# Optimization experiments

Hardware: AMD Instinct MI355X
Metric: run time of the kernel (lower is better)

## Reference

```python
import jax, jax.numpy as jnp
import numpy as np

B, C, H, W = 4, 256, 64, 64
DQK = C // 4


def setup_inputs() -> dict:
    key = jax.random.key(0)
    ks = jax.random.split(key, 5)
    s = 0.05
    x = jax.random.normal(ks[0], (B, C, H, W), dtype=jnp.float32)
    Wq = jax.random.normal(ks[1], (DQK, C), dtype=jnp.float32) * s
    Wk = jax.random.normal(ks[2], (DQK, C), dtype=jnp.float32) * s
    Wv = jax.random.normal(ks[3], (C, C), dtype=jnp.float32) * s
    bq = jnp.zeros((DQK,), jnp.float32)
    bk = jnp.zeros((DQK,), jnp.float32)
    bv = jnp.zeros((C,), jnp.float32)
    gamma = jnp.zeros((1,), jnp.float32)
    return {"x": x, "Wq": Wq, "bq": bq, "Wk": Wk, "bk": bk,
            "Wv": Wv, "bv": bv, "gamma": gamma}


def reference(x, Wq, bq, Wk, bk, Wv, bv, gamma):
    b, c, h, w = x.shape
    n = h * w
    xf = x.reshape(b, c, n)                      # [B, C, N]
    # 1x1 convs == per-pixel linear projections
    q = jnp.einsum('dc,bcn->bnd', Wq, xf) + bq   # [B, N, Dqk]
    k = jnp.einsum('dc,bcn->bdn', Wk, xf) + bk[None, :, None]  # [B, Dqk, N]
    v = jnp.einsum('ec,bcn->ben', Wv, xf) + bv[None, :, None]  # [B, C, N]
    energy = jnp.einsum('bnd,bdm->bnm', q, k)    # [B, N, N]
    attn = jax.nn.softmax(energy, axis=-1)       # softmax over keys
    # out[b,c,i] = sum_j v[b,c,j] * attn[b,i,j]
    out = jnp.einsum('bcj,bij->bci', v, attn)    # [B, C, N]
    out = out.reshape(b, c, h, w)
    return gamma * out + x
```

## Files before the change

kernel.cpp:

```cpp
#include <hip/hip_runtime.h>

#define B_ 4
#define C_ 256
#define N_ 4096
#define D_ 64

typedef __bf16 bf16x8 __attribute__((ext_vector_type(8)));
typedef float floatx4 __attribute__((ext_vector_type(4)));
typedef unsigned short ushort8v __attribute__((ext_vector_type(8)));
typedef unsigned short ushort4v __attribute__((ext_vector_type(4)));
typedef unsigned short ushort2v __attribute__((ext_vector_type(2)));

static __device__ __forceinline__ unsigned short f2bf(float f) {
    unsigned int u = __builtin_bit_cast(unsigned int, f);
    u += 0x7fffu + ((u >> 16) & 1u);
    return (unsigned short)(u >> 16);
}
static __device__ __forceinline__ float bf2f(unsigned short h) {
    unsigned int u = ((unsigned int)h) << 16;
    return __builtin_bit_cast(float, u);
}
static __device__ __forceinline__ unsigned int cvt_pk_bf16(float lo, float hi) {
    unsigned int d;
    asm("v_cvt_pk_bf16_f32 %0, %1, %2" : "=v"(d) : "v"(lo), "v"(hi));
    return d;
}

#define GLOAD16(gp, lp)                                                      \
    __builtin_amdgcn_global_load_lds(                                        \
        (const __attribute__((address_space(1))) void*)(gp),                 \
        (__attribute__((address_space(3))) void*)(lp), 16, 0, 0)

__global__ __launch_bounds__(256, 2) void proj_kernel(
    const float* __restrict__ x,
    const float* __restrict__ Wq, const float* __restrict__ Wk,
    const float* __restrict__ Wv,
    const float* __restrict__ bq, const float* __restrict__ bk,
    const float* __restrict__ bv,
    unsigned short* __restrict__ Qg, unsigned short* __restrict__ Kg,
    unsigned short* __restrict__ Vg)
{
    __shared__ __align__(16) unsigned short xs[64 * 264];
    __shared__ __align__(16) unsigned short Lt[128 * 72];

    const int n0 = blockIdx.x * 64;
    const int b  = blockIdx.y;
    const int t  = threadIdx.x;
    const int w  = t >> 6;
    const int lane = t & 63;
    const int g  = lane >> 4;
    const int m  = lane & 15;

#pragma unroll
    for (int k = 0; k < 8; ++k) {
        int e  = t + 256 * k;
        int cp = e >> 4;
        int c  = 2 * cp;
        int n4 = (e & 15) * 4;
        float4 v0 = *(const float4*)(x + ((size_t)b*C_ + c    )*N_ + n0 + n4);
        float4 v1 = *(const float4*)(x + ((size_t)b*C_ + c + 1)*N_ + n0 + n4);
        float a0[4] = {v0.x, v0.y, v0.z, v0.w};
        float a1[4] = {v1.x, v1.y, v1.z, v1.w};
#pragma unroll
        for (int j = 0; j < 4; ++j) {
            int n = n4 + j;
            unsigned int u = cvt_pk_bf16(a0[j], a1[j]);
            *(unsigned int*)&xs[n*264 + (((c >> 3) ^ (n & 7)) << 3) + (c & 7)] = u;
        }
    }
    __syncthreads();

#pragma unroll
    for (int s = 0; s < 3; ++s) {
        const int f0 = 128 * s;

        float bias_[2][4];
#pragma unroll
        for (int mt = 0; mt < 2; ++mt)
#pragma unroll
            for (int r = 0; r < 4; ++r) {
                int fg = f0 + 32*w + 16*mt + 4*g + r;
                bias_[mt][r] = (fg < 64) ? bq[fg]
                             : (fg < 128) ? bk[fg - 64] : bv[fg - 128];
            }

        const int fr0 = f0 + 32*w + m;
        const int fr1 = fr0 + 16;
        const float* wr0 = (fr0 < 64) ? Wq + (size_t)fr0*C_
                         : (fr0 < 128)? Wk + (size_t)(fr0 - 64)*C_
                                      : Wv + (size_t)(fr0 - 128)*C_;
        const float* wr1 = (fr1 < 64) ? Wq + (size_t)fr1*C_
                         : (fr1 < 128)? Wk + (size_t)(fr1 - 64)*C_
                                      : Wv + (size_t)(fr1 - 128)*C_;
        bf16x8 afr[2][8];
#pragma unroll
        for (int ks = 0; ks < 8; ++ks) {
            float4 l0 = *(const float4*)(wr0 + 32*ks + 8*g);
            float4 h0 = *(const float4*)(wr0 + 32*ks + 8*g + 4);
            float4 l1 = *(const float4*)(wr1 + 32*ks + 8*g);
            float4 h1 = *(const float4*)(wr1 + 32*ks + 8*g + 4);
            uint4 u0, u1;
            u0.x = cvt_pk_bf16(l0.x, l0.y); u0.y = cvt_pk_bf16(l0.z, l0.w);
            u0.z = cvt_pk_bf16(h0.x, h0.y); u0.w = cvt_pk_bf16(h0.z, h0.w);
            u1.x = cvt_pk_bf16(l1.x, l1.y); u1.y = cvt_pk_bf16(l1.z, l1.w);
            u1.z = cvt_pk_bf16(h1.x, h1.y); u1.w = cvt_pk_bf16(h1.z, h1.w);
            afr[0][ks] = __builtin_bit_cast(bf16x8, u0);
            afr[1][ks] = __builtin_bit_cast(bf16x8, u1);
        }

        floatx4 acc[2][4];
#pragma unroll
        for (int mt = 0; mt < 2; ++mt)
#pragma unroll
            for (int nt = 0; nt < 4; ++nt)
                acc[mt][nt] = (floatx4){0.f,0.f,0.f,0.f};

#pragma unroll
        for (int ks = 0; ks < 8; ++ks) {
#pragma unroll
            for (int nt = 0; nt < 4; ++nt) {
                int n = 16*nt + m;
                bf16x8 bfr = *(const bf16x8*)
                    &xs[n*264 + (((4*ks + g) ^ (n & 7)) << 3)];
#pragma unroll
                for (int mt = 0; mt < 2; ++mt)
                    acc[mt][nt] = __builtin_amdgcn_mfma_f32_16x16x32_bf16(
                                      afr[mt][ks], bfr, acc[mt][nt], 0, 0, 0);
            }
        }

#pragma unroll
        for (int mt = 0; mt < 2; ++mt)
#pragma unroll
            for (int nt = 0; nt < 4; ++nt)
#pragma unroll
                for (int r = 0; r < 4; ++r)
                    Lt[(32*w + 16*mt + 4*g + r)*72 + 16*nt + m] =
                        f2bf(acc[mt][nt][r] + bias_[mt][r]);
        __syncthreads();

        if (s == 0) {
#pragma unroll
            for (int k = 0; k < 4; ++k) {
                int e   = t + 256 * k;
                int fq0 = (e >> 6) * 8;
                int nl  = e & 63;
                ushort8v u;
#pragma unroll
                for (int j = 0; j < 8; ++j) u[j] = Lt[(fq0 + j)*72 + nl];
                unsigned short* dst = (fq0 < 64)
                    ? (Qg + ((size_t)b*N_ + n0 + nl)*D_ + fq0)
                    : (Kg + ((size_t)b*N_ + n0 + nl)*D_ + (fq0 - 64));
                *(ushort8v*)dst = u;
            }
        } else {
            const int cb = (s - 1) * 128;
#pragma unroll
            for (int k = 0; k < 4; ++k) {
                int e  = t + 256 * k;
                int fr = e >> 3;
                int n8 = (e & 7) * 8;
                ushort8v u = *(const ushort8v*)&Lt[fr*72 + n8];
                *(ushort8v*)(Vg + ((size_t)b*C_ + cb + fr)*N_ + n0 + n8) = u;
            }
        }
        __syncthreads();
    }
}

__global__ __launch_bounds__(512, 2) void flash_kernel(
    const unsigned short* __restrict__ Qg, const unsigned short* __restrict__ Kg,
    const unsigned short* __restrict__ Vg,
    unsigned short* __restrict__ Opart, float* __restrict__ ML)
{
    __shared__ __align__(16) unsigned short Vlds[32 * 512];
    __shared__ __align__(16) unsigned short Klds[2][8 * 512];
    __shared__ __align__(16) unsigned short PA[16 * 64 * 8];
    __shared__ float AL[128];

    const int g8   = blockIdx.x;
    const int tile = blockIdx.y;
    const int half = g8 & 1;
    const int b    = g8 >> 1;
    const int n0   = tile * 128;
    const int t    = threadIdx.x;
    const int w    = t >> 6;
    const int lane = t & 63;
    const int g    = lane >> 4;
    const int m    = lane & 15;
    const int wq   = w >> 2;
    const int cq   = w & 3;

    const unsigned short* Qb = Qg + ((size_t)b*N_ + n0)*D_;
    const unsigned short* Kb = Kg + (size_t)b*N_*D_;
    const unsigned short* Vb = Vg + (size_t)b*C_*N_;

    const int cstart = half * 32;
    const int cend   = cstart + 32;

    bf16x8 qf[2];
#pragma unroll
    for (int ks = 0; ks < 2; ++ks)
        qf[ks] = *(const bf16x8*)(Qb + (size_t)(16*w + m)*D_ + 32*ks + 8*g);

    floatx4 accO[4][4];
#pragma unroll
    for (int rt = 0; rt < 4; ++rt)
#pragma unroll
        for (int ct = 0; ct < 4; ++ct)
            accO[rt][ct] = (floatx4){0.f, 0.f, 0.f, 0.f};

    float mrow = -1e30f, lrow = 0.f;

    {
        const unsigned short* gp =
            Kb + (size_t)(cstart*64 + 16*(w >> 1) + m)*D_ + 32*(w & 1) + 8*g;
        GLOAD16(gp, &Klds[0][w * 512]);
    }
    __syncthreads();

    for (int t64 = cstart; t64 < cend; ++t64) {
        const int j0 = t64 * 64;
        const int kb = (t64 - cstart) & 1;

#pragma unroll
        for (int u = 0; u < 4; ++u) {
            int sidx = 4*w + u;
            int ks   = sidx >> 4;
            int cb   = sidx & 15;
            const unsigned short* gp =
                Vb + (size_t)(16*cb + m)*N_ + j0 + 32*ks + 8*g;
            GLOAD16(gp, &Vlds[sidx * 512]);
        }
        if (t64 + 1 < cend) {
            const unsigned short* gp =
                Kb + (size_t)((t64+1)*64 + 16*(w >> 1) + m)*D_
                   + 32*(w & 1) + 8*g;
            GLOAD16(gp, &Klds[kb ^ 1][w * 512]);
        }

        floatx4 accST[4];
#pragma unroll
        for (int jt = 0; jt < 4; ++jt) accST[jt] = (floatx4){0.f,0.f,0.f,0.f};
#pragma unroll
        for (int ks = 0; ks < 2; ++ks)
#pragma unroll
            for (int jt = 0; jt < 4; ++jt) {
                bf16x8 kfr = *(const bf16x8*)
                    &Klds[kb][(jt*2 + ks)*512 + lane*8];
                accST[jt] = __builtin_amdgcn_mfma_f32_16x16x32_bf16(
                                kfr, qf[ks], accST[jt], 0, 0, 0);
            }

        float mx = -1e30f;
#pragma unroll
        for (int jt = 0; jt < 4; ++jt)
#pragma unroll
            for (int r = 0; r < 4; ++r) mx = fmaxf(mx, accST[jt][r]);
        mx = fmaxf(mx, __shfl_xor(mx, 16));
        mx = fmaxf(mx, __shfl_xor(mx, 32));
        float mnew  = fmaxf(mrow, mx);
        float alpha = __expf(mrow - mnew);
        mrow = mnew;
        float p[4][4];
        float rs = 0.f;
#pragma unroll
        for (int jt = 0; jt < 4; ++jt)
#pragma unroll
            for (int r = 0; r < 4; ++r) {
                float e = __expf(accST[jt][r] - mnew);
                p[jt][r] = e;
                rs += e;
            }
        rs += __shfl_xor(rs, 16);
        rs += __shfl_xor(rs, 32);
        lrow = lrow * alpha + rs;

        if (g == 0) AL[16*w + m] = alpha;

#pragma unroll
        for (int jt = 0; jt < 4; ++jt) {
            uint2 pu;
            pu.x = cvt_pk_bf16(p[jt][0], p[jt][1]);
            pu.y = cvt_pk_bf16(p[jt][2], p[jt][3]);
            int frag = (w*2 + (jt >> 1))*64 + 16*(2*(jt & 1) + (g >> 1)) + m;
            *(uint2*)&PA[frag*8 + 4*(g & 1)] = pu;
        }

        __syncthreads();

#pragma unroll
        for (int rt = 0; rt < 4; ++rt) {
            floatx4 a4 = *(const floatx4*)&AL[64*wq + 16*rt + 4*g];
#pragma unroll
            for (int ct = 0; ct < 4; ++ct)
                accO[rt][ct] *= a4;
        }
#pragma unroll
        for (int ks = 0; ks < 2; ++ks) {
            bf16x8 pf[4];
#pragma unroll
            for (int rt = 0; rt < 4; ++rt)
                pf[rt] = *(const bf16x8*)
                    &PA[((8*wq + rt*2 + ks)*64 + lane)*8];
#pragma unroll
            for (int ct = 0; ct < 4; ++ct) {
                int sidx = ks*16 + 4*cq + ct;
                bf16x8 vfrag = *(const bf16x8*)&Vlds[sidx*512 + lane*8];
#pragma unroll
                for (int rt = 0; rt < 4; ++rt)
                    accO[rt][ct] = __builtin_amdgcn_mfma_f32_16x16x32_bf16(
                                       pf[rt], vfrag, accO[rt][ct], 0, 0, 0);
            }
        }

        __syncthreads();
    }

    const size_t tbase = ((size_t)(half*B_ + b)*32 + tile);
    unsigned short* Ob = Opart + tbase * (C_ * 128);
    float* ml = ML + tbase * 256;

    if (g == 0) {
        ml[16*w + m]       = mrow;
        ml[128 + 16*w + m] = lrow;
    }

#pragma unroll
    for (int rt = 0; rt < 4; ++rt)
#pragma unroll
        for (int ct = 0; ct < 4; ++ct) {
            int c  = 64*cq + 16*ct + m;
            int q0 = 64*wq + 16*rt + 4*g;
            uint2 pu;
            pu.x = cvt_pk_bf16(accO[rt][ct][0], accO[rt][ct][1]);
            pu.y = cvt_pk_bf16(accO[rt][ct][2], accO[rt][ct][3]);
            *(uint2*)(Ob + (size_t)c*128 + q0) = pu;
        }
}

__global__ __launch_bounds__(256) void combine_kernel(
    const unsigned short* __restrict__ Opart, const float* __restrict__ ML,
    const float* __restrict__ x, const float* __restrict__ gamma,
    float* __restrict__ out)
{
    __shared__ float sc0[128], sc1[128];
    const int tile   = blockIdx.x;
    const int cslice = blockIdx.y;
    const int b      = blockIdx.z;
    const int n0     = tile * 128;
    const int t      = threadIdx.x;

    if (t < 128) {
        const float* ml0 = ML + ((size_t)(0*B_ + b)*32 + tile)*256;
        const float* ml1 = ML + ((size_t)(1*B_ + b)*32 + tile)*256;
        float m0 = ml0[t], l0 = ml0[128 + t];
        float m1 = ml1[t], l1 = ml1[128 + t];
        float M  = fmaxf(m0, m1);
        float f0 = __expf(m0 - M), f1 = __expf(m1 - M);
        float L  = f0*l0 + f1*l1;
        float gm = gamma[0];
        sc0[t] = gm * f0 / L;
        sc1[t] = gm * f1 / L;
    }
    __syncthreads();

    const int nq = t & 31;
    const int cl = t >> 5;
    const float* xb = x   + (size_t)b*C_*N_;
    float*       ob = out + (size_t)b*C_*N_;
    const unsigned short* O0 = Opart + ((size_t)(0*B_ + b)*32 + tile)*(C_*128);
    const unsigned short* O1 = Opart + ((size_t)(1*B_ + b)*32 + tile)*(C_*128);

    float s0[4], s1[4];
#pragma unroll
    for (int k = 0; k < 4; ++k) { s0[k] = sc0[4*nq + k]; s1[k] = sc1[4*nq + k]; }

#pragma unroll
    for (int i = 0; i < 4; ++i) {
        int c = 32*cslice + 8*i + cl;
        float4 x4 = *(const float4*)(xb + (size_t)c*N_ + n0 + 4*nq);
        ushort4v a4 = *(const ushort4v*)(O0 + (size_t)c*128 + 4*nq);
        ushort4v b4 = *(const ushort4v*)(O1 + (size_t)c*128 + 4*nq);
        float4 y;
        y.x = s0[0]*bf2f(a4[0]) + s1[0]*bf2f(b4[0]) + x4.x;
        y.y = s0[1]*bf2f(a4[1]) + s1[1]*bf2f(b4[1]) + x4.y;
        y.z = s0[2]*bf2f(a4[2]) + s1[2]*bf2f(b4[2]) + x4.z;
        y.w = s0[3]*bf2f(a4[3]) + s1[3]*bf2f(b4[3]) + x4.w;
        *(float4*)(ob + (size_t)c*N_ + n0 + 4*nq) = y;
    }
}

extern "C" void kernel_launch(void* const* d_in, const int* in_sizes, int n_in,
                              void* d_out, int out_size, void* d_ws, size_t ws_size,
                              hipStream_t stream) {
    const float* x     = (const float*)d_in[0];
    const float* Wq    = (const float*)d_in[1];
    const float* bq    = (const float*)d_in[2];
    const float* Wk    = (const float*)d_in[3];
    const float* bk    = (const float*)d_in[4];
    const float* Wv    = (const float*)d_in[5];
    const float* bv    = (const float*)d_in[6];
    const float* gamma = (const float*)d_in[7];
    float* out = (float*)d_out;

    unsigned short* Qg = (unsigned short*)d_ws;
    unsigned short* Kg = Qg + (size_t)B_*N_*D_;
    unsigned short* Vg = Kg + (size_t)B_*N_*D_;
    unsigned short* Op = Vg + (size_t)B_*C_*N_;
    float* ML = (float*)(Op + (size_t)2*B_*32*C_*128);

    proj_kernel<<<dim3(64, 4), 256, 0, stream>>>(x, Wq, Wk, Wv,
                                                 bq, bk, bv, Qg, Kg, Vg);
    flash_kernel<<<dim3(8, 32), 512, 0, stream>>>(Qg, Kg, Vg, Op, ML);
    combine_kernel<<<dim3(32, 8, 4), 256, 0, stream>>>(Op, ML, x, gamma, out);
}
```

Baseline: 186.9 us.

## Rework flash attention with 32x32 MFMA tiles, 4-way key split, double-buffered V

```diff
diff --git a/kernel.cpp b/kernel.cpp
--- a/kernel.cpp
+++ b/kernel.cpp
@@ -7,6 +7,7 @@
 
 typedef __bf16 bf16x8 __attribute__((ext_vector_type(8)));
 typedef float floatx4 __attribute__((ext_vector_type(4)));
+typedef float floatx16 __attribute__((ext_vector_type(16)));
 typedef unsigned short ushort8v __attribute__((ext_vector_type(8)));
 typedef unsigned short ushort4v __attribute__((ext_vector_type(4)));
 typedef unsigned short ushort2v __attribute__((ext_vector_type(2)));
@@ -31,7 +32,7 @@
         (const __attribute__((address_space(1))) void*)(gp),                 \
         (__attribute__((address_space(3))) void*)(lp), 16, 0, 0)
 
-__global__ __launch_bounds__(256, 2) void proj_kernel(
+__global__ __launch_bounds__(256, 3) void proj_kernel(
     const float* __restrict__ x,
     const float* __restrict__ Wq, const float* __restrict__ Wk,
     const float* __restrict__ Wv,
@@ -40,11 +41,13 @@
     unsigned short* __restrict__ Qg, unsigned short* __restrict__ Kg,
     unsigned short* __restrict__ Vg)
 {
-    __shared__ __align__(16) unsigned short xs[64 * 264];
-    __shared__ __align__(16) unsigned short Lt[128 * 72];
+    __shared__ __align__(16) unsigned short smem[64 * 264];
+    unsigned short* xs = smem;
+    unsigned short* Lt = smem;
 
     const int n0 = blockIdx.x * 64;
-    const int b  = blockIdx.y;
+    const int f0 = blockIdx.y * 128;
+    const int b  = blockIdx.z;
     const int t  = threadIdx.x;
     const int w  = t >> 6;
     const int lane = t & 63;
@@ -68,103 +71,99 @@
             *(unsigned int*)&xs[n*264 + (((c >> 3) ^ (n & 7)) << 3) + (c & 7)] = u;
         }
     }
+
+    float bias_[2][4];
+#pragma unroll
+    for (int mt = 0; mt < 2; ++mt)
+#pragma unroll
+        for (int r = 0; r < 4; ++r) {
+            int fg = f0 + 32*w + 16*mt + 4*g + r;
+            bias_[mt][r] = (fg < 64) ? bq[fg]
+                         : (fg < 128) ? bk[fg - 64] : bv[fg - 128];
+        }
+
+    const int fr0 = f0 + 32*w + m;
+    const int fr1 = fr0 + 16;
+    const float* wr0 = (fr0 < 64) ? Wq + (size_t)fr0*C_
+                     : (fr0 < 128)? Wk + (size_t)(fr0 - 64)*C_
+                                  : Wv + (size_t)(fr0 - 128)*C_;
+    const float* wr1 = (fr1 < 64) ? Wq + (size_t)fr1*C_
+                     : (fr1 < 128)? Wk + (size_t)(fr1 - 64)*C_
+                                  : Wv + (size_t)(fr1 - 128)*C_;
+    bf16x8 afr[2][8];
+#pragma unroll
+    for (int ks = 0; ks < 8; ++ks) {
+        float4 l0 = *(const float4*)(wr0 + 32*ks + 8*g);
+        float4 h0 = *(const float4*)(wr0 + 32*ks + 8*g + 4);
+        float4 l1 = *(const float4*)(wr1 + 32*ks + 8*g);
+        float4 h1 = *(const float4*)(wr1 + 32*ks + 8*g + 4);
+        uint4 u0, u1;
+        u0.x = cvt_pk_bf16(l0.x, l0.y); u0.y = cvt_pk_bf16(l0.z, l0.w);
+        u0.z = cvt_pk_bf16(h0.x, h0.y); u0.w = cvt_pk_bf16(h0.z, h0.w);
+        u1.x = cvt_pk_bf16(l1.x, l1.y); u1.y = cvt_pk_bf16(l1.z, l1.w);
+        u1.z = cvt_pk_bf16(h1.x, h1.y); u1.w = cvt_pk_bf16(h1.z, h1.w);
+        afr[0][ks] = __builtin_bit_cast(bf16x8, u0);
+        afr[1][ks] = __builtin_bit_cast(bf16x8, u1);
+    }
+
+    floatx4 acc[2][4];
+#pragma unroll
+    for (int mt = 0; mt < 2; ++mt)
+#pragma unroll
+        for (int nt = 0; nt < 4; ++nt) acc[mt][nt] = (floatx4){0.f,0.f,0.f,0.f};
+
     __syncthreads();
 
 #pragma unroll
-    for (int s = 0; s < 3; ++s) {
-        const int f0 = 128 * s;
-
-        float bias_[2][4];
-#pragma unroll
-        for (int mt = 0; mt < 2; ++mt)
-#pragma unroll
-            for (int r = 0; r < 4; ++r) {
-                int fg = f0 + 32*w + 16*mt + 4*g + r;
-                bias_[mt][r] = (fg < 64) ? bq[fg]
-                             : (fg < 128) ? bk[fg - 64] : bv[fg - 128];
-            }
-
-        const int fr0 = f0 + 32*w + m;
-        const int fr1 = fr0 + 16;
-        const float* wr0 = (fr0 < 64) ? Wq + (size_t)fr0*C_
-                         : (fr0 < 128)? Wk + (size_t)(fr0 - 64)*C_
-                                      : Wv + (size_t)(fr0 - 128)*C_;
-        const float* wr1 = (fr1 < 64) ? Wq + (size_t)fr1*C_
-                         : (fr1 < 128)? Wk + (size_t)(fr1 - 64)*C_
-                                      : Wv + (size_t)(fr1 - 128)*C_;
-        bf16x8 afr[2][8];
-#pragma unroll
-        for (int ks = 0; ks < 8; ++ks) {
-            float4 l0 = *(const float4*)(wr0 + 32*ks + 8*g);
-            float4 h0 = *(const float4*)(wr0 + 32*ks + 8*g + 4);
-            float4 l1 = *(const float4*)(wr1 + 32*ks + 8*g);
-            float4 h1 = *(const float4*)(wr1 + 32*ks + 8*g + 4);
-            uint4 u0, u1;
-            u0.x = cvt_pk_bf16(l0.x, l0.y); u0.y = cvt_pk_bf16(l0.z, l0.w);
-            u0.z = cvt_pk_bf16(h0.x, h0.y); u0.w = cvt_pk_bf16(h0.z, h0.w);
-            u1.x = cvt_pk_bf16(l1.x, l1.y); u1.y = cvt_pk_bf16(l1.z, l1.w);
-            u1.z = cvt_pk_bf16(h1.x, h1.y); u1.w = cvt_pk_bf16(h1.z, h1.w);
-            afr[0][ks] = __builtin_bit_cast(bf16x8, u0);
-            afr[1][ks] = __builtin_bit_cast(bf16x8, u1);
-        }
-
-        floatx4 acc[2][4];
-#pragma unroll
-        for (int mt = 0; mt < 2; ++mt)
-#pragma unroll
-            for (int nt = 0; nt < 4; ++nt)
-                acc[mt][nt] = (floatx4){0.f,0.f,0.f,0.f};
-
-#pragma unroll
-        for (int ks = 0; ks < 8; ++ks) {
-#pragma unroll
-            for (int nt = 0; nt < 4; ++nt) {
-                int n = 16*nt + m;
-                bf16x8 bfr = *(const bf16x8*)
-                    &xs[n*264 + (((4*ks + g) ^ (n & 7)) << 3)];
-#pragma unroll
-                for (int mt = 0; mt < 2; ++mt)
-                    acc[mt][nt] = __builtin_amdgcn_mfma_f32_16x16x32_bf16(
-                                      afr[mt][ks], bfr, acc[mt][nt], 0, 0, 0);
-            }
-        }
-
-#pragma unroll
-        for (int mt = 0; mt < 2; ++mt)
-#pragma unroll
-            for (int nt = 0; nt < 4; ++nt)
-#pragma unroll
-                for (int r = 0; r < 4; ++r)
-                    Lt[(32*w + 16*mt + 4*g + r)*72 + 16*nt + m] =
-                        f2bf(acc[mt][nt][r] + bias_[mt][r]);
-        __syncthreads();
-
-        if (s == 0) {
-#pragma unroll
-            for (int k = 0; k < 4; ++k) {
-                int e   = t + 256 * k;
-                int fq0 = (e >> 6) * 8;
-                int nl  = e & 63;
-                ushort8v u;
-#pragma unroll
-                for (int j = 0; j < 8; ++j) u[j] = Lt[(fq0 + j)*72 + nl];
-                unsigned short* dst = (fq0 < 64)
-                    ? (Qg + ((size_t)b*N_ + n0 + nl)*D_ + fq0)
-                    : (Kg + ((size_t)b*N_ + n0 + nl)*D_ + (fq0 - 64));
-                *(ushort8v*)dst = u;
-            }
-        } else {
-            const int cb = (s - 1) * 128;
-#pragma unroll
-            for (int k = 0; k < 4; ++k) {
-                int e  = t + 256 * k;
-                int fr = e >> 3;
-                int n8 = (e & 7) * 8;
-                ushort8v u = *(const ushort8v*)&Lt[fr*72 + n8];
-                *(ushort8v*)(Vg + ((size_t)b*C_ + cb + fr)*N_ + n0 + n8) = u;
-            }
-        }
-        __syncthreads();
+    for (int ks = 0; ks < 8; ++ks) {
+#pragma unroll
+        for (int nt = 0; nt < 4; ++nt) {
+            int n = 16*nt + m;
+            bf16x8 bfr = *(const bf16x8*)
+                &xs[n*264 + (((4*ks + g) ^ (n & 7)) << 3)];
+#pragma unroll
+            for (int mt = 0; mt < 2; ++mt)
+                acc[mt][nt] = __builtin_amdgcn_mfma_f32_16x16x32_bf16(
+                                  afr[mt][ks], bfr, acc[mt][nt], 0, 0, 0);
+        }
+    }
+
+    __syncthreads();
+
+#pragma unroll
+    for (int mt = 0; mt < 2; ++mt)
+#pragma unroll
+        for (int nt = 0; nt < 4; ++nt)
+#pragma unroll
+            for (int r = 0; r < 4; ++r)
+                Lt[(32*w + 16*mt + 4*g + r)*72 + 16*nt + m] =
+                    f2bf(acc[mt][nt][r] + bias_[mt][r]);
+    __syncthreads();
+
+    if (f0 == 0) {
+#pragma unroll
+        for (int k = 0; k < 4; ++k) {
+            int e   = t + 256 * k;
+            int fq0 = (e >> 6) * 8;
+            int nl  = e & 63;
+            ushort8v u;
+#pragma unroll
+            for (int j = 0; j < 8; ++j) u[j] = Lt[(fq0 + j)*72 + nl];
+            unsigned short* dst = (fq0 < 64)
+                ? (Qg + ((size_t)b*N_ + n0 + nl)*D_ + fq0)
+                : (Kg + ((size_t)b*N_ + n0 + nl)*D_ + (fq0 - 64));
+            *(ushort8v*)dst = u;
+        }
+    } else {
+        const int cb = f0 - 128;
+#pragma unroll
+        for (int k = 0; k < 4; ++k) {
+            int e  = t + 256 * k;
+            int fr = e >> 3;
+            int n8 = (e & 7) * 8;
+            ushort8v u = *(const ushort8v*)&Lt[fr*72 + n8];
+            *(ushort8v*)(Vg + ((size_t)b*C_ + cb + fr)*N_ + n0 + n8) = u;
+        }
     }
 }
 
@@ -173,170 +172,170 @@
     const unsigned short* __restrict__ Vg,
     unsigned short* __restrict__ Opart, float* __restrict__ ML)
 {
-    __shared__ __align__(16) unsigned short Vlds[32 * 512];
+    __shared__ __align__(16) unsigned short Vlds[2][32 * 512];
     __shared__ __align__(16) unsigned short Klds[2][8 * 512];
-    __shared__ __align__(16) unsigned short PA[16 * 64 * 8];
-    __shared__ float AL[128];
-
-    const int g8   = blockIdx.x;
+    __shared__ float AL[8][32];
+
+    const int gx   = blockIdx.x;
     const int tile = blockIdx.y;
-    const int half = g8 & 1;
-    const int b    = g8 >> 1;
-    const int n0   = tile * 128;
+    const int quarter = gx & 3;
+    const int b    = gx >> 2;
+    const int n0   = tile * 256;
     const int t    = threadIdx.x;
     const int w    = t >> 6;
     const int lane = t & 63;
-    const int g    = lane >> 4;
-    const int m    = lane & 15;
-    const int wq   = w >> 2;
-    const int cq   = w & 3;
+    const int q32  = lane & 31;
+    const int h    = lane >> 5;
 
     const unsigned short* Qb = Qg + ((size_t)b*N_ + n0)*D_;
     const unsigned short* Kb = Kg + (size_t)b*N_*D_;
     const unsigned short* Vb = Vg + (size_t)b*C_*N_;
 
-    const int cstart = half * 32;
-    const int cend   = cstart + 32;
-
-    bf16x8 qf[2];
-#pragma unroll
-    for (int ks = 0; ks < 2; ++ks)
-        qf[ks] = *(const bf16x8*)(Qb + (size_t)(16*w + m)*D_ + 32*ks + 8*g);
-
-    floatx4 accO[4][4];
-#pragma unroll
-    for (int rt = 0; rt < 4; ++rt)
-#pragma unroll
-        for (int ct = 0; ct < 4; ++ct)
-            accO[rt][ct] = (floatx4){0.f, 0.f, 0.f, 0.f};
+    const int cstart = quarter * 16;
+    const int cend   = cstart + 16;
+
+    bf16x8 qf[4];
+#pragma unroll
+    for (int ks = 0; ks < 4; ++ks)
+        qf[ks] = *(const bf16x8*)(Qb + (size_t)(32*w + q32)*D_ + 16*ks + 8*h);
+
+    floatx16 accO[8];
+#pragma unroll
+    for (int ct = 0; ct < 8; ++ct)
+#pragma unroll
+        for (int r = 0; r < 16; ++r) accO[ct][r] = 0.f;
 
     float mrow = -1e30f, lrow = 0.f;
 
-    {
-        const unsigned short* gp =
-            Kb + (size_t)(cstart*64 + 16*(w >> 1) + m)*D_ + 32*(w & 1) + 8*g;
-        GLOAD16(gp, &Klds[0][w * 512]);
-    }
+#define STAGE_K(T64, BUF) do {                                               \
+    const unsigned short* gp = Kb                                            \
+        + (size_t)((T64)*64 + 32*(w >> 2) + q32)*D_ + 16*(w & 3) + 8*h;      \
+    GLOAD16(gp, &Klds[BUF][w * 512]); } while (0)
+
+#define STAGE_V(T64, BUF) do {                                               \
+    _Pragma("unroll")                                                        \
+    for (int u_ = 0; u_ < 4; ++u_) {                                         \
+        const unsigned short* gp = Vb                                        \
+            + (size_t)(32*w + q32)*N_ + (T64)*64 + 16*u_ + 8*h;              \
+        GLOAD16(gp, &Vlds[BUF][(w*4 + u_) * 512]);                           \
+    } } while (0)
+
+    STAGE_K(cstart, 0);
+    STAGE_V(cstart, 0);
     __syncthreads();
 
     for (int t64 = cstart; t64 < cend; ++t64) {
-        const int j0 = t64 * 64;
-        const int kb = (t64 - cstart) & 1;
-
-#pragma unroll
-        for (int u = 0; u < 4; ++u) {
-            int sidx = 4*w + u;
-            int ks   = sidx >> 4;
-            int cb   = sidx & 15;
-            const unsigned short* gp =
-                Vb + (size_t)(16*cb + m)*N_ + j0 + 32*ks + 8*g;
-            GLOAD16(gp, &Vlds[sidx * 512]);
-        }
+        const int cur = (t64 - cstart) & 1;
+
         if (t64 + 1 < cend) {
-            const unsigned short* gp =
-                Kb + (size_t)((t64+1)*64 + 16*(w >> 1) + m)*D_
-                   + 32*(w & 1) + 8*g;
-            GLOAD16(gp, &Klds[kb ^ 1][w * 512]);
-        }
-
-        floatx4 accST[4];
-#pragma unroll
-        for (int jt = 0; jt < 4; ++jt) accST[jt] = (floatx4){0.f,0.f,0.f,0.f};
-#pragma unroll
-        for (int ks = 0; ks < 2; ++ks)
-#pragma unroll
-            for (int jt = 0; jt < 4; ++jt) {
+            STAGE_K(t64 + 1, cur ^ 1);
+            STAGE_V(t64 + 1, cur ^ 1);
+        }
+
+        floatx16 accS[2];
+#pragma unroll
+        for (int kt = 0; kt < 2; ++kt)
+#pragma unroll
+            for (int r = 0; r < 16; ++r) accS[kt][r] = 0.f;
+#pragma unroll
+        for (int kt = 0; kt < 2; ++kt)
+#pragma unroll
+            for (int ks = 0; ks < 4; ++ks) {
                 bf16x8 kfr = *(const bf16x8*)
-                    &Klds[kb][(jt*2 + ks)*512 + lane*8];
-                accST[jt] = __builtin_amdgcn_mfma_f32_16x16x32_bf16(
-                                kfr, qf[ks], accST[jt], 0, 0, 0);
+                    &Klds[cur][(kt*4 + ks)*512 + lane*8];
+                accS[kt] = __builtin_amdgcn_mfma_f32_32x32x16_bf16(
+                               kfr, qf[ks], accS[kt], 0, 0, 0);
             }
 
         float mx = -1e30f;
 #pragma unroll
-        for (int jt = 0; jt < 4; ++jt)
-#pragma unroll
-            for (int r = 0; r < 4; ++r) mx = fmaxf(mx, accST[jt][r]);
-        mx = fmaxf(mx, __shfl_xor(mx, 16));
+        for (int kt = 0; kt < 2; ++kt)
+#pragma unroll
+            for (int r = 0; r < 16; ++r) mx = fmaxf(mx, accS[kt][r]);
         mx = fmaxf(mx, __shfl_xor(mx, 32));
         float mnew  = fmaxf(mrow, mx);
         float alpha = __expf(mrow - mnew);
         mrow = mnew;
-        float p[4][4];
+        float p[2][16];
         float rs = 0.f;
 #pragma unroll
-        for (int jt = 0; jt < 4; ++jt)
-#pragma unroll
-            for (int r = 0; r < 4; ++r) {
-                float e = __expf(accST[jt][r] - mnew);
-                p[jt][r] = e;
+        for (int kt = 0; kt < 2; ++kt)
+#pragma unroll
+            for (int r = 0; r < 16; ++r) {
+                float e = __expf(accS[kt][r] - mnew);
+                p[kt][r] = e;
                 rs += e;
             }
-        rs += __shfl_xor(rs, 16);
         rs += __shfl_xor(rs, 32);
         lrow = lrow * alpha + rs;
-
-        if (g == 0) AL[16*w + m] = alpha;
-
-#pragma unroll
-        for (int jt = 0; jt < 4; ++jt) {
+        if (h == 0) AL[w][q32] = alpha;
+
+        bf16x8 pa[4];
+#pragma unroll
+        for (int kt = 0; kt < 2; ++kt)
+#pragma unroll
+            for (int cp = 0; cp < 2; ++cp) {
+                unsigned int Y0 = cvt_pk_bf16(p[kt][8*cp + 0], p[kt][8*cp + 1]);
+                unsigned int Y1 = cvt_pk_bf16(p[kt][8*cp + 2], p[kt][8*cp + 3]);
+                unsigned int X0 = cvt_pk_bf16(p[kt][8*cp + 4], p[kt][8*cp + 5]);
+                unsigned int X1 = cvt_pk_bf16(p[kt][8*cp + 6], p[kt][8*cp + 7]);
+                asm volatile("v_permlane32_swap_b32 %0, %1"
+                             : "+v"(Y0), "+v"(X0));
+                asm volatile("v_permlane32_swap_b32 %0, %1"
+                             : "+v"(Y1), "+v"(X1));
+                uint4 fu; fu.x = Y0; fu.y = Y1; fu.z = X0; fu.w = X1;
+                pa[kt*2 + cp] = __builtin_bit_cast(bf16x8, fu);
+            }
+
+        float4 av[4];
+#pragma unroll
+        for (int gp = 0; gp < 4; ++gp)
+            av[gp] = *(const float4*)&AL[w][8*gp + 4*h];
+#pragma unroll
+        for (int ct = 0; ct < 8; ++ct)
+#pragma unroll
+            for (int gp = 0; gp < 4; ++gp)
+#pragma unroll
+                for (int i = 0; i < 4; ++i)
+                    accO[ct][4*gp + i] *= av[gp][i];
+
+        __builtin_amdgcn_s_setprio(1);
+#pragma unroll
+        for (int ct = 0; ct < 8; ++ct)
+#pragma unroll
+            for (int kc = 0; kc < 4; ++kc) {
+                bf16x8 vf = *(const bf16x8*)
+                    &Vlds[cur][(ct*4 + kc)*512 + lane*8];
+                accO[ct] = __builtin_amdgcn_mfma_f32_32x32x16_bf16(
+                               pa[kc], vf, accO[ct], 0, 0, 0);
+            }
+        __builtin_amdgcn_s_setprio(0);
+
+        __syncthreads();
+    }
+
+    const size_t tbase = ((size_t)(quarter*B_ + b)*16 + tile);
+    unsigned short* Ob = Opart + tbase * (C_ * 256);
+    float* ml = ML + tbase * 512;
+
+    if (h == 0) {
+        ml[32*w + q32]       = mrow;
+        ml[256 + 32*w + q32] = lrow;
+    }
+
+#pragma unroll
+    for (int ct = 0; ct < 8; ++ct) {
+        int c = 32*ct + q32;
+#pragma unroll
+        for (int gp = 0; gp < 4; ++gp) {
             uint2 pu;
-            pu.x = cvt_pk_bf16(p[jt][0], p[jt][1]);
-            pu.y = cvt_pk_bf16(p[jt][2], p[jt][3]);
-            int frag = (w*2 + (jt >> 1))*64 + 16*(2*(jt & 1) + (g >> 1)) + m;
-            *(uint2*)&PA[frag*8 + 4*(g & 1)] = pu;
-        }
-
-        __syncthreads();
-
-#pragma unroll
-        for (int rt = 0; rt < 4; ++rt) {
-            floatx4 a4 = *(const floatx4*)&AL[64*wq + 16*rt + 4*g];
-#pragma unroll
-            for (int ct = 0; ct < 4; ++ct)
-                accO[rt][ct] *= a4;
-        }
-#pragma unroll
-        for (int ks = 0; ks < 2; ++ks) {
-            bf16x8 pf[4];
-#pragma unroll
-            for (int rt = 0; rt < 4; ++rt)
-                pf[rt] = *(const bf16x8*)
-                    &PA[((8*wq + rt*2 + ks)*64 + lane)*8];
-#pragma unroll
-            for (int ct = 0; ct < 4; ++ct) {
-                int sidx = ks*16 + 4*cq + ct;
-                bf16x8 vfrag = *(const bf16x8*)&Vlds[sidx*512 + lane*8];
-#pragma unroll
-                for (int rt = 0; rt < 4; ++rt)
-                    accO[rt][ct] = __builtin_amdgcn_mfma_f32_16x16x32_bf16(
-                                       pf[rt], vfrag, accO[rt][ct], 0, 0, 0);
-            }
-        }
-
-        __syncthreads();
-    }
-
-    const size_t tbase = ((size_t)(half*B_ + b)*32 + tile);
-    unsigned short* Ob = Opart + tbase * (C_ * 128);
-    float* ml = ML + tbase * 256;
-
-    if (g == 0) {
-        ml[16*w + m]       = mrow;
-        ml[128 + 16*w + m] = lrow;
-    }
-
-#pragma unroll
-    for (int rt = 0; rt < 4; ++rt)
-#pragma unroll
-        for (int ct = 0; ct < 4; ++ct) {
-            int c  = 64*cq + 16*ct + m;
-            int q0 = 64*wq + 16*rt + 4*g;
-            uint2 pu;
-            pu.x = cvt_pk_bf16(accO[rt][ct][0], accO[rt][ct][1]);
-            pu.y = cvt_pk_bf16(accO[rt][ct][2], accO[rt][ct][3]);
-            *(uint2*)(Ob + (size_t)c*128 + q0) = pu;
-        }
+            pu.x = cvt_pk_bf16(accO[ct][4*gp + 0], accO[ct][4*gp + 1]);
+            pu.y = cvt_pk_bf16(accO[ct][4*gp + 2], accO[ct][4*gp + 3]);
+            *(uint2*)(Ob + (size_t)c*256 + 32*w + 8*gp + 4*h) = pu;
+        }
+    }
+#undef STAGE_K
+#undef STAGE_V
 }
 
 __global__ __launch_bounds__(256) void combine_kernel(
@@ -344,49 +343,61 @@
     const float* __restrict__ x, const float* __restrict__ gamma,
     float* __restrict__ out)
 {
-    __shared__ float sc0[128], sc1[128];
+    __shared__ float sc[4][256];
     const int tile   = blockIdx.x;
     const int cslice = blockIdx.y;
     const int b      = blockIdx.z;
-    const int n0     = tile * 128;
+    const int n0     = tile * 256;
     const int t      = threadIdx.x;
 
-    if (t < 128) {
-        const float* ml0 = ML + ((size_t)(0*B_ + b)*32 + tile)*256;
-        const float* ml1 = ML + ((size_t)(1*B_ + b)*32 + tile)*256;
-        float m0 = ml0[t], l0 = ml0[128 + t];
-        float m1 = ml1[t], l1 = ml1[128 + t];
-        float M  = fmaxf(m0, m1);
-        float f0 = __expf(m0 - M), f1 = __expf(m1 - M);
-        float L  = f0*l0 + f1*l1;
+    {
+        float mm[4], ll[4];
+        float M = -1e30f;
+#pragma unroll
+        for (int s = 0; s < 4; ++s) {
+            const float* mls = ML + ((size_t)(s*B_ + b)*16 + tile)*512;
+            mm[s] = mls[t];
+            ll[s] = mls[256 + t];
+            M = fmaxf(M, mm[s]);
+        }
+        float fs[4];
+        float L = 0.f;
+#pragma unroll
+        for (int s = 0; s < 4; ++s) { fs[s] = __expf(mm[s] - M); L += fs[s]*ll[s]; }
         float gm = gamma[0];
-        sc0[t] = gm * f0 / L;
-        sc1[t] = gm * f1 / L;
+#pragma unroll
+        for (int s = 0; s < 4; ++s) sc[s][t] = gm * fs[s] / L;
     }
     __syncthreads();
 
-    const int nq = t & 31;
-    const int cl = t >> 5;
+    const int nq = t & 63;
+    const int cl = t >> 6;
     const float* xb = x   + (size_t)b*C_*N_;
     float*       ob = out + (size_t)b*C_*N_;
-    const unsigned short* O0 = Opart + ((size_t)(0*B_ + b)*32 + tile)*(C_*128);
-    const unsigned short* O1 = Opart + ((size_t)(1*B_ + b)*32 + tile)*(C_*128);
-
-    float s0[4], s1[4];
-#pragma unroll
-    for (int k = 0; k < 4; ++k) { s0[k] = sc0[4*nq + k]; s1[k] = sc1[4*nq + k]; }
-
-#pragma unroll
-    for (int i = 0; i < 4; ++i) {
-        int c = 32*cslice + 8*i + cl;
+    const unsigned short* Os[4];
+#pragma unroll
+    for (int s = 0; s < 4; ++s)
+        Os[s] = Opart + ((size_t)(s*B_ + b)*16 + tile)*(C_*256);
+
+    float sv[4][4];
+#pragma unroll
+    for (int s = 0; s < 4; ++s)
+#pragma unroll
+        for (int k = 0; k < 4; ++k) sv[s][k] = sc[s][4*nq + k];
+
+#pragma unroll
+    for (int i = 0; i < 8; ++i) {
+        int c = 32*cslice + 4*i + cl;
         float4 x4 = *(const float4*)(xb + (size_t)c*N_ + n0 + 4*nq);
-        ushort4v a4 = *(const ushort4v*)(O0 + (size_t)c*128 + 4*nq);
-        ushort4v b4 = *(const ushort4v*)(O1 + (size_t)c*128 + 4*nq);
-        float4 y;
-        y.x = s0[0]*bf2f(a4[0]) + s1[0]*bf2f(b4[0]) + x4.x;
-        y.y = s0[1]*bf2f(a4[1]) + s1[1]*bf2f(b4[1]) + x4.y;
-        y.z = s0[2]*bf2f(a4[2]) + s1[2]*bf2f(b4[2]) + x4.z;
-        y.w = s0[3]*bf2f(a4[3]) + s1[3]*bf2f(b4[3]) + x4.w;
+        float4 y = x4;
+#pragma unroll
+        for (int s = 0; s < 4; ++s) {
+            ushort4v a4 = *(const ushort4v*)(Os[s] + (size_t)c*256 + 4*nq);
+            y.x += sv[s][0]*bf2f(a4[0]);
+            y.y += sv[s][1]*bf2f(a4[1]);
+            y.z += sv[s][2]*bf2f(a4[2]);
+            y.w += sv[s][3]*bf2f(a4[3]);
+        }
         *(float4*)(ob + (size_t)c*N_ + n0 + 4*nq) = y;
     }
 }
@@ -408,10 +419,10 @@
     unsigned short* Kg = Qg + (size_t)B_*N_*D_;
     unsigned short* Vg = Kg + (size_t)B_*N_*D_;
     unsigned short* Op = Vg + (size_t)B_*C_*N_;
-    float* ML = (float*)(Op + (size_t)2*B_*32*C_*128);
-
-    proj_kernel<<<dim3(64, 4), 256, 0, stream>>>(x, Wq, Wk, Wv,
-                                                 bq, bk, bv, Qg, Kg, Vg);
-    flash_kernel<<<dim3(8, 32), 512, 0, stream>>>(Qg, Kg, Vg, Op, ML);
-    combine_kernel<<<dim3(32, 8, 4), 256, 0, stream>>>(Op, ML, x, gamma, out);
-}
+    float* ML = (float*)(Op + (size_t)4*B_*16*C_*256);
+
+    proj_kernel<<<dim3(64, 3, 4), 256, 0, stream>>>(x, Wq, Wk, Wv,
+                                                    bq, bk, bv, Qg, Kg, Vg);
+    flash_kernel<<<dim3(16, 16), 512, 0, stream>>>(Qg, Kg, Vg, Op, ML);
+    combine_kernel<<<dim3(16, 8, 4), 256, 0, stream>>>(Op, ML, x, gamma, out);
+}
```

Result: faster. 173.1 us (-7.4%).
